# Performance work log

Hardware: AMD Instinct MI355X
Metric: run time of the kernel (lower is better)

Reference implementation:

```python
import jax, jax.numpy as jnp
import numpy as np

B, HEADS, HEAD_DIM, WS = 64, 6, 32, 8
POS_DIM = 12  # (dim//4)//4 = 192//16
N = WS ** 3


def _ln(x, g, b, eps=1e-5):
    mu = jnp.mean(x, axis=-1, keepdims=True)
    var = jnp.var(x, axis=-1, keepdims=True)
    return (x - mu) / jnp.sqrt(var + eps) * g + b


def setup_inputs() -> dict:
    key = jax.random.key(0)
    ks = jax.random.split(key, 10)
    s = 0.02
    inp = {
        'q': jax.random.normal(ks[0], (B, HEADS, N, HEAD_DIM), jnp.float32),
        'k': jax.random.normal(ks[1], (B, HEADS, N, HEAD_DIM), jnp.float32),
        'v': jax.random.normal(ks[2], (B, HEADS, N, HEAD_DIM), jnp.float32),
        'h': WS, 'w': WS, 'd': WS,
        'pos_proj_w': jax.random.normal(ks[3], (3, POS_DIM), jnp.float32) * s,
        'pos_proj_b': jnp.zeros((POS_DIM,), jnp.float32),
        'ln1_g': jnp.ones((POS_DIM,), jnp.float32),
        'ln1_b': jnp.zeros((POS_DIM,), jnp.float32),
        'w1': jax.random.normal(ks[4], (POS_DIM, POS_DIM), jnp.float32) * s,
        'b1': jnp.zeros((POS_DIM,), jnp.float32),
        'ln2_g': jnp.ones((POS_DIM,), jnp.float32),
        'ln2_b': jnp.zeros((POS_DIM,), jnp.float32),
        'w2': jax.random.normal(ks[5], (POS_DIM, POS_DIM), jnp.float32) * s,
        'b2': jnp.zeros((POS_DIM,), jnp.float32),
        'ln3_g': jnp.ones((POS_DIM,), jnp.float32),
        'ln3_b': jnp.zeros((POS_DIM,), jnp.float32),
        'w3': jax.random.normal(ks[6], (POS_DIM, HEADS), jnp.float32) * s,
        'b3': jnp.zeros((HEADS,), jnp.float32),
    }
    return inp


def reference(q, k, v, h, w, d,
              pos_proj_w, pos_proj_b,
              ln1_g, ln1_b, w1, b1,
              ln2_g, ln2_b, w2, b2,
              ln3_g, ln3_b, w3, b3):
    scale = HEAD_DIM ** (-0.5)
    attn = jnp.einsum('bhnc,bhmc->bhnm', q * scale, k)

    # candidate relative offsets table: ((2h-1)(2w-1)(2d-1), 3)
    bh = jnp.arange(1 - h, h, dtype=jnp.float32)
    bw = jnp.arange(1 - w, w, dtype=jnp.float32)
    bd = jnp.arange(1 - d, d, dtype=jnp.float32)
    biases = jnp.stack(jnp.meshgrid(bh, bw, bd, indexing='ij')).reshape(3, -1).T

    # per-pair relative index (faithfully sums the 3 shifted coords, as source does)
    coords = jnp.stack(jnp.meshgrid(jnp.arange(h), jnp.arange(w), jnp.arange(d),
                                    indexing='ij')).reshape(3, -1)  # (3, N)
    rel = coords[:, :, None] - coords[:, None, :]  # (3, N, N)
    rel_idx = (rel[0] + h - 1) + (rel[1] + w - 1) + (rel[2] + d - 1)  # (N, N)

    # dynamic pos-bias MLP
    x = biases @ pos_proj_w + pos_proj_b
    x = jax.nn.relu(_ln(x, ln1_g, ln1_b)) @ w1 + b1
    x = jax.nn.relu(_ln(x, ln2_g, ln2_b)) @ w2 + b2
    pos = jax.nn.relu(_ln(x, ln3_g, ln3_b)) @ w3 + b3  # (table, heads)

    rpb = pos[rel_idx]                       # (N, N, heads) gather
    attn = attn + jnp.transpose(rpb, (2, 0, 1))[None]  # (1, heads, N, N)

    attn = jax.nn.softmax(attn, axis=-1)
    return jnp.einsum('bhnm,bhmc->bhnc', attn, v)
```

## Files before the change

### kernel.cpp

```cpp
#include <hip/hip_runtime.h>
#include <math.h>

typedef _Float16 h8 __attribute__((ext_vector_type(8)));
typedef _Float16 h4 __attribute__((ext_vector_type(4)));
typedef float    f4 __attribute__((ext_vector_type(4)));

#define NHEADS 6
#define HDIM   32
#define NTOK   512
#define NTAB   43
#define LOG2E  1.44269504088896340736f

#define FRAG_BYTES (64L * NHEADS * 32 * 64 * 8 * 2)
#define OFF_Q 4096L
#define OFF_K (OFF_Q + FRAG_BYTES)
#define OFF_V (OFF_K + FRAG_BYTES)

__device__ inline int ds3(int x) {
  return (x >> 6) + ((x >> 3) & 7) + (x & 7);
}

__device__ inline void ln_relu12(const float* x, float* t, const float* g, const float* b) {
  float mu = 0.f;
#pragma unroll
  for (int j = 0; j < 12; j++) mu += x[j];
  mu *= (1.f / 12.f);
  float var = 0.f;
#pragma unroll
  for (int j = 0; j < 12; j++) { float d = x[j] - mu; var += d * d; }
  var *= (1.f / 12.f);
  float inv = rsqrtf(var + 1e-5f);
#pragma unroll
  for (int j = 0; j < 12; j++) {
    float y = (x[j] - mu) * inv * g[j] + b[j];
    t[j] = y > 0.f ? y : 0.f;
  }
}

__device__ inline void mm12(const float* t, float* x, const float* w, const float* c) {
#pragma unroll
  for (int j = 0; j < 12; j++) {
    float acc = c[j];
#pragma unroll
    for (int i = 0; i < 12; i++) acc += t[i] * w[i * 12 + j];
    x[j] = acc;
  }
}

__global__ void pos_mlp_kernel(
    const float* __restrict__ pw, const float* __restrict__ pb,
    const float* __restrict__ g1, const float* __restrict__ b1,
    const float* __restrict__ w1, const float* __restrict__ c1,
    const float* __restrict__ g2, const float* __restrict__ b2,
    const float* __restrict__ w2, const float* __restrict__ c2,
    const float* __restrict__ g3, const float* __restrict__ b3,
    const float* __restrict__ w3, const float* __restrict__ c3,
    float* __restrict__ posb)
{
  const int r = threadIdx.x;
  if (r >= NTAB) return;
  const float bh = -7.0f;
  const float bw = (float)(r / 15) - 7.0f;
  const float bd = (float)(r % 15) - 7.0f;
  float x[12], t[12];
#pragma unroll
  for (int j = 0; j < 12; j++)
    x[j] = bh * pw[j] + bw * pw[12 + j] + bd * pw[24 + j] + pb[j];
  ln_relu12(x, t, g1, b1); mm12(t, x, w1, c1);
  ln_relu12(x, t, g2, b2); mm12(t, x, w2, c2);
  ln_relu12(x, t, g3, b3);
#pragma unroll
  for (int hd = 0; hd < NHEADS; hd++) {
    float acc = c3[hd];
#pragma unroll
    for (int i = 0; i < 12; i++) acc += t[i] * w3[i * NHEADS + hd];
    posb[r * NHEADS + hd] = acc * LOG2E;
  }
}

__global__ __launch_bounds__(256)
void prepack_kernel(const float* __restrict__ q, const float* __restrict__ k,
                    const float* __restrict__ v, _Float16* __restrict__ Qf,
                    _Float16* __restrict__ Kf, _Float16* __restrict__ Vf)
{
  __shared__ _Float16 Qs[64 * 40];
  __shared__ _Float16 Ks[64 * 40];
  __shared__ _Float16 Vt[32 * 72];

  const float SC = 0.17677669529663687f * LOG2E;

  const int tid = threadIdx.x;
  const int c   = blockIdx.x;
  const int bh  = blockIdx.z * NHEADS + blockIdx.y;
  const long base = (long)bh * NTOK * HDIM + (long)c * 64 * HDIM;
  const float4* qg = (const float4*)(q + base);
  const float4* kg = (const float4*)(k + base);
  const float4* vg = (const float4*)(v + base);

#pragma unroll
  for (int i = 0; i < 2; i++) {
    int f = i * 256 + tid;
    int row = f >> 3, c4 = f & 7;
    float4 a = qg[f];
    h4 ah = { (_Float16)(a.x * SC), (_Float16)(a.y * SC),
              (_Float16)(a.z * SC), (_Float16)(a.w * SC) };
    *(h4*)&Qs[row * 40 + c4 * 4] = ah;
    float4 e = kg[f];
    h4 eh = { (_Float16)e.x, (_Float16)e.y, (_Float16)e.z, (_Float16)e.w };
    *(h4*)&Ks[row * 40 + c4 * 4] = eh;
    float4 w = vg[f];
    Vt[(c4 * 4 + 0) * 72 + row] = (_Float16)w.x;
    Vt[(c4 * 4 + 1) * 72 + row] = (_Float16)w.y;
    Vt[(c4 * 4 + 2) * 72 + row] = (_Float16)w.z;
    Vt[(c4 * 4 + 3) * 72 + row] = (_Float16)w.w;
  }
  __syncthreads();

  const int lane = tid & 63, t = tid >> 6;
  const int quad = lane >> 4, l16 = lane & 15;
  const long fo = ((long)(bh * 32 + c * 4 + t) * 64 + lane) * 8;

  *(h8*)(Qf + fo) = *(const h8*)&Qs[(t * 16 + l16) * 40 + quad * 8];
  *(h8*)(Kf + fo) = *(const h8*)&Ks[(t * 16 + l16) * 40 + quad * 8];
  *(h8*)(Vf + fo) = *(const h8*)&Vt[((t & 1) * 16 + l16) * 72 + (t >> 1) * 32 + quad * 8];
}

__global__ __launch_bounds__(256, 4)
void attn_kernel(const _Float16* __restrict__ Qf, const _Float16* __restrict__ Kf,
                 const _Float16* __restrict__ Vf, const float* __restrict__ posb,
                 float* __restrict__ out)
{
  __shared__ _Float16 Pt[4][2][16 * 72];
  __shared__ float    Os[4][16 * 36];
  __shared__ f4       posw4r[NTAB];

  const int tid  = threadIdx.x;
  const int wave = tid >> 6;
  const int lane = tid & 63;
  const int quad = lane >> 4;
  const int l16  = lane & 15;
  const int h    = blockIdx.y;
  const int bh   = blockIdx.z * NHEADS + h;

  if (tid >= 3 && tid < NTAB) {
    f4 pv = { posb[tid * NHEADS + h],       posb[(tid - 1) * NHEADS + h],
              posb[(tid - 2) * NHEADS + h], posb[(tid - 3) * NHEADS + h] };
    posw4r[tid] = pv;
  }
  __syncthreads();

  const int qt = blockIdx.x * 4 + wave;
  const h8 qf = *(const h8*)(Qf + ((long)(bh * 32 + qt) * 64 + lane) * 8);
  const int qs21 = ds3(qt * 16) + (l16 >> 3) + (l16 & 7) + 21;
  const int kdq  = (quad >> 1) + (quad & 1) * 4;

  f4 o0 = {0.f, 0.f, 0.f, 0.f};
  f4 o1 = {0.f, 0.f, 0.f, 0.f};
  float lp = 0.f;

  const _Float16* kbase = Kf + ((long)bh * 32 * 64 + lane) * 8;
  const _Float16* vbase = Vf + ((long)bh * 32 * 64 + lane) * 8;

#pragma unroll
  for (int kc = 0; kc < 8; kc++) {
    h8 kf[4], vf[4];
#pragma unroll
    for (int t = 0; t < 4; t++) {
      kf[t] = *(const h8*)(kbase + (kc * 4 + t) * 64 * 8);
      vf[t] = *(const h8*)(vbase + (kc * 4 + t) * 64 * 8);
    }

    f4 s[4];
#pragma unroll
    for (int t = 0; t < 4; t++) {
      int idx0 = qs21 - (kc + t * 2 + kdq);
      f4 cin = posw4r[idx0];
      s[t] = __builtin_amdgcn_mfma_f32_16x16x32_f16(kf[t], qf, cin, 0, 0, 0);
    }

    _Float16* pt = &Pt[wave][kc & 1][0];
#pragma unroll
    for (int t = 0; t < 4; t++) {
      float p0 = __builtin_amdgcn_exp2f(s[t][0]);
      float p1 = __builtin_amdgcn_exp2f(s[t][1]);
      float p2 = __builtin_amdgcn_exp2f(s[t][2]);
      float p3 = __builtin_amdgcn_exp2f(s[t][3]);
      lp += (p0 + p1) + (p2 + p3);
      h4 hv = { (_Float16)p0, (_Float16)p1, (_Float16)p2, (_Float16)p3 };
      *(h4*)&pt[l16 * 72 + t * 16 + quad * 4] = hv;
    }

#pragma unroll
    for (int kt = 0; kt < 2; kt++) {
      h8 pf = *(const h8*)&pt[l16 * 72 + kt * 32 + quad * 8];
      o0 = __builtin_amdgcn_mfma_f32_16x16x32_f16(vf[kt * 2 + 0], pf, o0, 0, 0, 0);
      o1 = __builtin_amdgcn_mfma_f32_16x16x32_f16(vf[kt * 2 + 1], pf, o1, 0, 0, 0);
    }
  }

  lp += __shfl_xor(lp, 16);
  lp += __shfl_xor(lp, 32);
  const float inv = 1.f / lp;
  float* os = &Os[wave][0];
  f4 w0 = { o0[0] * inv, o0[1] * inv, o0[2] * inv, o0[3] * inv };
  f4 w1 = { o1[0] * inv, o1[1] * inv, o1[2] * inv, o1[3] * inv };
  *(f4*)&os[l16 * 36 + quad * 4]      = w0;
  *(f4*)&os[l16 * 36 + 16 + quad * 4] = w1;
  const int q_ = lane >> 2, seg = lane & 3;
  f4 r0 = *(const f4*)&os[q_ * 36 + seg * 8];
  f4 r1 = *(const f4*)&os[q_ * 36 + seg * 8 + 4];
  float* orow = out + (long)bh * NTOK * HDIM + (long)(qt * 16 + q_) * HDIM + seg * 8;
  *(float4*)orow       = *(float4*)&r0;
  *(float4*)(orow + 4) = *(float4*)&r1;
}

extern "C" void kernel_launch(void* const* d_in, const int* in_sizes, int n_in,
                              void* d_out, int out_size, void* d_ws, size_t ws_size,
                              hipStream_t stream) {
  (void)in_sizes; (void)n_in; (void)out_size; (void)ws_size;
  const float* q  = (const float*)d_in[0];
  const float* k  = (const float*)d_in[1];
  const float* v  = (const float*)d_in[2];
  const float* pw  = (const float*)d_in[6];
  const float* pb  = (const float*)d_in[7];
  const float* g1  = (const float*)d_in[8];
  const float* b1  = (const float*)d_in[9];
  const float* w1  = (const float*)d_in[10];
  const float* c1  = (const float*)d_in[11];
  const float* g2  = (const float*)d_in[12];
  const float* b2  = (const float*)d_in[13];
  const float* w2  = (const float*)d_in[14];
  const float* c2  = (const float*)d_in[15];
  const float* g3  = (const float*)d_in[16];
  const float* b3  = (const float*)d_in[17];
  const float* w3  = (const float*)d_in[18];
  const float* c3  = (const float*)d_in[19];

  char* ws = (char*)d_ws;
  float*     posb = (float*)ws;
  _Float16*  Qf   = (_Float16*)(ws + OFF_Q);
  _Float16*  Kf   = (_Float16*)(ws + OFF_K);
  _Float16*  Vf   = (_Float16*)(ws + OFF_V);
  float* outp = (float*)d_out;

  pos_mlp_kernel<<<1, 64, 0, stream>>>(pw, pb, g1, b1, w1, c1, g2, b2, w2, c2,
                                       g3, b3, w3, c3, posb);
  prepack_kernel<<<dim3(8, NHEADS, 64), 256, 0, stream>>>(q, k, v, Qf, Kf, Vf);
  attn_kernel<<<dim3(8, NHEADS, 64), 256, 0, stream>>>(Qf, Kf, Vf, posb, outp);
}
```

Before: 194.3 us.

## Fuse pos-MLP into prepack and give each attention wave two query tiles

Removes the separate single-block pos-MLP launch by computing the bias table inside block (0,0,0) of the prepack kernel. The attention kernel now has each wave process two 16-row query tiles, so every K/V fragment load feeds twice the MFMA work and the grid shrinks to 384x4 blocks ordered by batch-head. Shared P and O buffers are merged into one reused scratch region. The costs are higher register pressure and half as many blocks. Dropping the double-buffered P tile (kc&1) also removes the separation between consecutive iterations' LDS writes and reads.

After: 165.6 us. 1.17x faster.

```diff
diff --git a/kernel.cpp b/kernel.cpp
--- a/kernel.cpp
+++ b/kernel.cpp
@@ -47,49 +47,46 @@
   }
 }
 
-__global__ void pos_mlp_kernel(
-    const float* __restrict__ pw, const float* __restrict__ pb,
-    const float* __restrict__ g1, const float* __restrict__ b1,
-    const float* __restrict__ w1, const float* __restrict__ c1,
-    const float* __restrict__ g2, const float* __restrict__ b2,
-    const float* __restrict__ w2, const float* __restrict__ c2,
-    const float* __restrict__ g3, const float* __restrict__ b3,
-    const float* __restrict__ w3, const float* __restrict__ c3,
-    float* __restrict__ posb)
-{
-  const int r = threadIdx.x;
-  if (r >= NTAB) return;
-  const float bh = -7.0f;
-  const float bw = (float)(r / 15) - 7.0f;
-  const float bd = (float)(r % 15) - 7.0f;
-  float x[12], t[12];
-#pragma unroll
-  for (int j = 0; j < 12; j++)
-    x[j] = bh * pw[j] + bw * pw[12 + j] + bd * pw[24 + j] + pb[j];
-  ln_relu12(x, t, g1, b1); mm12(t, x, w1, c1);
-  ln_relu12(x, t, g2, b2); mm12(t, x, w2, c2);
-  ln_relu12(x, t, g3, b3);
-#pragma unroll
-  for (int hd = 0; hd < NHEADS; hd++) {
-    float acc = c3[hd];
-#pragma unroll
-    for (int i = 0; i < 12; i++) acc += t[i] * w3[i * NHEADS + hd];
-    posb[r * NHEADS + hd] = acc * LOG2E;
-  }
-}
-
 __global__ __launch_bounds__(256)
 void prepack_kernel(const float* __restrict__ q, const float* __restrict__ k,
                     const float* __restrict__ v, _Float16* __restrict__ Qf,
-                    _Float16* __restrict__ Kf, _Float16* __restrict__ Vf)
+                    _Float16* __restrict__ Kf, _Float16* __restrict__ Vf,
+                    const float* __restrict__ pw, const float* __restrict__ pb,
+                    const float* __restrict__ g1, const float* __restrict__ b1,
+                    const float* __restrict__ w1, const float* __restrict__ c1,
+                    const float* __restrict__ g2, const float* __restrict__ b2,
+                    const float* __restrict__ w2, const float* __restrict__ c2,
+                    const float* __restrict__ g3, const float* __restrict__ b3,
+                    const float* __restrict__ w3, const float* __restrict__ c3,
+                    float* __restrict__ posb)
 {
   __shared__ _Float16 Qs[64 * 40];
   __shared__ _Float16 Ks[64 * 40];
   __shared__ _Float16 Vt[32 * 72];
 
   const float SC = 0.17677669529663687f * LOG2E;
-
   const int tid = threadIdx.x;
+
+  if (blockIdx.x == 0 && blockIdx.y == 0 && blockIdx.z == 0 && tid < NTAB) {
+    const float bh_ = -7.0f;
+    const float bw_ = (float)(tid / 15) - 7.0f;
+    const float bd_ = (float)(tid % 15) - 7.0f;
+    float x[12], t[12];
+#pragma unroll
+    for (int j = 0; j < 12; j++)
+      x[j] = bh_ * pw[j] + bw_ * pw[12 + j] + bd_ * pw[24 + j] + pb[j];
+    ln_relu12(x, t, g1, b1); mm12(t, x, w1, c1);
+    ln_relu12(x, t, g2, b2); mm12(t, x, w2, c2);
+    ln_relu12(x, t, g3, b3);
+#pragma unroll
+    for (int hd = 0; hd < NHEADS; hd++) {
+      float acc = c3[hd];
+#pragma unroll
+      for (int i = 0; i < 12; i++) acc += t[i] * w3[i * NHEADS + hd];
+      posb[tid * NHEADS + hd] = acc * LOG2E;
+    }
+  }
+
   const int c   = blockIdx.x;
   const int bh  = blockIdx.z * NHEADS + blockIdx.y;
   const long base = (long)bh * NTOK * HDIM + (long)c * 64 * HDIM;
@@ -130,17 +127,17 @@
                  const _Float16* __restrict__ Vf, const float* __restrict__ posb,
                  float* __restrict__ out)
 {
-  __shared__ _Float16 Pt[4][2][16 * 72];
-  __shared__ float    Os[4][16 * 36];
-  __shared__ f4       posw4r[NTAB];
+  __shared__ __align__(16) char smem[4][2][2304];
+  __shared__ f4 posw4r[NTAB];
 
   const int tid  = threadIdx.x;
   const int wave = tid >> 6;
   const int lane = tid & 63;
   const int quad = lane >> 4;
   const int l16  = lane & 15;
-  const int h    = blockIdx.y;
-  const int bh   = blockIdx.z * NHEADS + h;
+  const int bh   = blockIdx.x;
+  const int h    = bh % NHEADS;
+  const int qq   = blockIdx.y;
 
   if (tid >= 3 && tid < NTAB) {
     f4 pv = { posb[tid * NHEADS + h],       posb[(tid - 1) * NHEADS + h],
@@ -149,14 +146,20 @@
   }
   __syncthreads();
 
-  const int qt = blockIdx.x * 4 + wave;
-  const h8 qf = *(const h8*)(Qf + ((long)(bh * 32 + qt) * 64 + lane) * 8);
-  const int qs21 = ds3(qt * 16) + (l16 >> 3) + (l16 & 7) + 21;
-  const int kdq  = (quad >> 1) + (quad & 1) * 4;
-
-  f4 o0 = {0.f, 0.f, 0.f, 0.f};
-  f4 o1 = {0.f, 0.f, 0.f, 0.f};
-  float lp = 0.f;
+  int qt[2] = { qq * 8 + wave * 2, qq * 8 + wave * 2 + 1 };
+  h8 qf[2];
+  int qs21[2];
+#pragma unroll
+  for (int ti = 0; ti < 2; ti++) {
+    qf[ti] = *(const h8*)(Qf + ((long)(bh * 32 + qt[ti]) * 64 + lane) * 8);
+    qs21[ti] = ds3(qt[ti] * 16) + (l16 >> 3) + (l16 & 7) + 21;
+  }
+  const int kdq = (quad >> 1) + (quad & 1) * 4;
+
+  f4 o[2][2];
+#pragma unroll
+  for (int ti = 0; ti < 2; ti++) { o[ti][0] = f4{0,0,0,0}; o[ti][1] = f4{0,0,0,0}; }
+  float lp[2] = {0.f, 0.f};
 
   const _Float16* kbase = Kf + ((long)bh * 32 * 64 + lane) * 8;
   const _Float16* vbase = Vf + ((long)bh * 32 * 64 + lane) * 8;
@@ -170,48 +173,53 @@
       vf[t] = *(const h8*)(vbase + (kc * 4 + t) * 64 * 8);
     }
 
-    f4 s[4];
-#pragma unroll
-    for (int t = 0; t < 4; t++) {
-      int idx0 = qs21 - (kc + t * 2 + kdq);
-      f4 cin = posw4r[idx0];
-      s[t] = __builtin_amdgcn_mfma_f32_16x16x32_f16(kf[t], qf, cin, 0, 0, 0);
+#pragma unroll
+    for (int ti = 0; ti < 2; ti++) {
+      _Float16* pt = (_Float16*)smem[wave][ti];
+      f4 s[4];
+#pragma unroll
+      for (int t = 0; t < 4; t++) {
+        int idx0 = qs21[ti] - (kc + t * 2 + kdq);
+        f4 cin = posw4r[idx0];
+        s[t] = __builtin_amdgcn_mfma_f32_16x16x32_f16(kf[t], qf[ti], cin, 0, 0, 0);
+      }
+#pragma unroll
+      for (int t = 0; t < 4; t++) {
+        float p0 = __builtin_amdgcn_exp2f(s[t][0]);
+        float p1 = __builtin_amdgcn_exp2f(s[t][1]);
+        float p2 = __builtin_amdgcn_exp2f(s[t][2]);
+        float p3 = __builtin_amdgcn_exp2f(s[t][3]);
+        lp[ti] += (p0 + p1) + (p2 + p3);
+        h4 hv = { (_Float16)p0, (_Float16)p1, (_Float16)p2, (_Float16)p3 };
+        *(h4*)&pt[l16 * 72 + t * 16 + quad * 4] = hv;
+      }
+#pragma unroll
+      for (int kt = 0; kt < 2; kt++) {
+        h8 pf = *(const h8*)&pt[l16 * 72 + kt * 32 + quad * 8];
+        o[ti][0] = __builtin_amdgcn_mfma_f32_16x16x32_f16(vf[kt * 2 + 0], pf, o[ti][0], 0, 0, 0);
+        o[ti][1] = __builtin_amdgcn_mfma_f32_16x16x32_f16(vf[kt * 2 + 1], pf, o[ti][1], 0, 0, 0);
+      }
     }
-
-    _Float16* pt = &Pt[wave][kc & 1][0];
-#pragma unroll
-    for (int t = 0; t < 4; t++) {
-      float p0 = __builtin_amdgcn_exp2f(s[t][0]);
-      float p1 = __builtin_amdgcn_exp2f(s[t][1]);
-      float p2 = __builtin_amdgcn_exp2f(s[t][2]);
-      float p3 = __builtin_amdgcn_exp2f(s[t][3]);
-      lp += (p0 + p1) + (p2 + p3);
-      h4 hv = { (_Float16)p0, (_Float16)p1, (_Float16)p2, (_Float16)p3 };
-      *(h4*)&pt[l16 * 72 + t * 16 + quad * 4] = hv;
-    }
-
-#pragma unroll
-    for (int kt = 0; kt < 2; kt++) {
-      h8 pf = *(const h8*)&pt[l16 * 72 + kt * 32 + quad * 8];
-      o0 = __builtin_amdgcn_mfma_f32_16x16x32_f16(vf[kt * 2 + 0], pf, o0, 0, 0, 0);
-      o1 = __builtin_amdgcn_mfma_f32_16x16x32_f16(vf[kt * 2 + 1], pf, o1, 0, 0, 0);
-    }
-  }
-
-  lp += __shfl_xor(lp, 16);
-  lp += __shfl_xor(lp, 32);
-  const float inv = 1.f / lp;
-  float* os = &Os[wave][0];
-  f4 w0 = { o0[0] * inv, o0[1] * inv, o0[2] * inv, o0[3] * inv };
-  f4 w1 = { o1[0] * inv, o1[1] * inv, o1[2] * inv, o1[3] * inv };
-  *(f4*)&os[l16 * 36 + quad * 4]      = w0;
-  *(f4*)&os[l16 * 36 + 16 + quad * 4] = w1;
-  const int q_ = lane >> 2, seg = lane & 3;
-  f4 r0 = *(const f4*)&os[q_ * 36 + seg * 8];
-  f4 r1 = *(const f4*)&os[q_ * 36 + seg * 8 + 4];
-  float* orow = out + (long)bh * NTOK * HDIM + (long)(qt * 16 + q_) * HDIM + seg * 8;
-  *(float4*)orow       = *(float4*)&r0;
-  *(float4*)(orow + 4) = *(float4*)&r1;
+  }
+
+#pragma unroll
+  for (int ti = 0; ti < 2; ti++) {
+    float l = lp[ti];
+    l += __shfl_xor(l, 16);
+    l += __shfl_xor(l, 32);
+    const float inv = 1.f / l;
+    float* os = (float*)smem[wave][ti];
+    f4 w0 = { o[ti][0][0] * inv, o[ti][0][1] * inv, o[ti][0][2] * inv, o[ti][0][3] * inv };
+    f4 w1 = { o[ti][1][0] * inv, o[ti][1][1] * inv, o[ti][1][2] * inv, o[ti][1][3] * inv };
+    *(f4*)&os[l16 * 36 + quad * 4]      = w0;
+    *(f4*)&os[l16 * 36 + 16 + quad * 4] = w1;
+    const int q_ = lane >> 2, seg = lane & 3;
+    f4 r0 = *(const f4*)&os[q_ * 36 + seg * 8];
+    f4 r1 = *(const f4*)&os[q_ * 36 + seg * 8 + 4];
+    float* orow = out + (long)bh * NTOK * HDIM + (long)(qt[ti] * 16 + q_) * HDIM + seg * 8;
+    *(float4*)orow       = *(float4*)&r0;
+    *(float4*)(orow + 4) = *(float4*)&r1;
+  }
 }
 
 extern "C" void kernel_launch(void* const* d_in, const int* in_sizes, int n_in,
@@ -243,8 +251,8 @@
   _Float16*  Vf   = (_Float16*)(ws + OFF_V);
   float* outp = (float*)d_out;
 
-  pos_mlp_kernel<<<1, 64, 0, stream>>>(pw, pb, g1, b1, w1, c1, g2, b2, w2, c2,
-                                       g3, b3, w3, c3, posb);
-  prepack_kernel<<<dim3(8, NHEADS, 64), 256, 0, stream>>>(q, k, v, Qf, Kf, Vf);
-  attn_kernel<<<dim3(8, NHEADS, 64), 256, 0, stream>>>(Qf, Kf, Vf, posb, outp);
-}
+  prepack_kernel<<<dim3(8, NHEADS, 64), 256, 0, stream>>>(
+      q, k, v, Qf, Kf, Vf,
+      pw, pb, g1, b1, w1, c1, g2, b2, w2, c2, g3, b3, w3, c3, posb);
+  attn_kernel<<<dim3(384, 4), 256, 0, stream>>>(Qf, Kf, Vf, posb, outp);
+}
```
